# Kernel tuning notes

Hardware: AMD Instinct MI355X
Metric: run time of the kernel (lower is better)

## Reference

```python
import jax, jax.numpy as jnp
import numpy as np

EMB = 300      # emb_size
SEQ = 100      # seq_len
KW = 5         # kernel_width
KN = 50        # kernel_num
KMAX = 3       # maxpooling_num
MLP1 = 75      # decoder_mlp1_num
VOCAB = 50000 + 2
B = 2048
QLEN = 5


def setup_inputs() -> dict:
    key = jax.random.key(0)
    ks = jax.random.split(key, 11)
    input_q = jax.random.randint(ks[0], (QLEN,), 0, 50000)
    input_d = jax.random.randint(ks[1], (B, SEQ), 0, 50000)
    emb_table = jax.random.normal(ks[2], (VOCAB, EMB), jnp.float32) * 0.1
    conv_w = jax.random.normal(ks[3], (KW, 3 * EMB, KN), jnp.float32) * 0.02  # WIO
    conv_b = jnp.zeros((KN,), jnp.float32)
    gate_w = jax.random.normal(ks[4], (EMB, KN), jnp.float32) * 0.05
    gate_b = jnp.zeros((KN,), jnp.float32)
    hid_w = jax.random.normal(ks[5], (KN * KMAX, MLP1), jnp.float32) * 0.05
    hid_b = jnp.zeros((MLP1,), jnp.float32)
    score_w = jax.random.normal(ks[6], (MLP1, 1), jnp.float32) * 0.05
    score_b = jnp.zeros((1,), jnp.float32)
    return {"input_q": input_q, "input_d": input_d, "emb_table": emb_table,
            "conv_w": conv_w, "conv_b": conv_b, "gate_w": gate_w, "gate_b": gate_b,
            "hid_w": hid_w, "hid_b": hid_b, "score_w": score_w, "score_b": score_b}


def kmax_pool(x, k):
    # x: [B, KN, L]; keep top-k values along last axis in original sequence order
    _, idx = jax.lax.top_k(x, k)
    idx = jnp.sort(idx, axis=-1)
    return jnp.take_along_axis(x, idx, axis=-1)  # [B, KN, k]


def reference(input_q, input_d, emb_table, conv_w, conv_b, gate_w, gate_b,
              hid_w, hid_b, score_w, score_b):
    # class vector: mean of query-word embeddings -> [EMB]
    class_vec = emb_table[input_q].mean(axis=0)
    # category-specific gate -> [KN]
    query_gate = jax.nn.sigmoid(class_vec @ gate_w + gate_b)
    # document embeddings -> [B, SEQ, EMB]
    emb = emb_table[input_d]
    # elementwise interaction features, concat -> [B, SEQ, 3*EMB]
    conv_in = jnp.concatenate([emb, class_vec * emb, class_vec - emb], axis=-1)
    # conv over sequence (full-width kernel == 1D conv with C_in=3*EMB) -> [B, SEQ-KW+1, KN]
    conv = jax.lax.conv_general_dilated(
        conv_in, conv_w, window_strides=(1,), padding='VALID',
        dimension_numbers=('NWC', 'WIO', 'NWC')) + conv_b
    gated = query_gate * conv                      # [B, L', KN]
    pooled = kmax_pool(jnp.swapaxes(gated, 1, 2), KMAX)  # [B, KN, KMAX]
    enc = pooled.reshape(pooled.shape[0], -1)      # [B, KN*KMAX] = [B, 150]
    mlp1 = jnp.tanh(enc @ hid_w + hid_b)           # [B, 75]
    score = jnp.tanh(mlp1 @ score_w + score_b)     # [B, 1]
    return (mlp1, score)
```

## Files before the change

### kernel.cpp

```cpp
#include <hip/hip_runtime.h>
#include <math.h>

#define EMB   300
#define SEQ   100
#define KW    5
#define KN    50
#define NPAD  64
#define KMAX  3
#define MLP1  75
#define LOUT  96
#define BATCH 2048
#define EPAD  320
#define CHW   32
#define NCHK  10
#define SPW   36
#define TAU   2.5e-6
#define WHA   0.75
#define WHB   0.25
#define FLAG_TAU 1e-5f

#define WS_C    0
#define WS_GATE 320
#define WS_BIAS 384
#define WS_WG   448
#define F64_DBL 96448
#define WH_F    0
#define WL_F    51200
#define ENC_OFF 102400
#define ENC_PITCH 152
#define FLAGCNT_OFF 413696
#define FLAGLIST_OFF 413704
#define FLAGCAP 4096

typedef __attribute__((ext_vector_type(8))) short short8;
typedef __attribute__((ext_vector_type(4))) float f32x4;

__device__ __forceinline__ unsigned pack_hl(float x) {
    unsigned u = __float_as_uint(x);
    unsigned hi = (u + 0x7fffu + ((u >> 16) & 1u)) >> 16;
    float r = x - __uint_as_float(hi << 16);
    unsigned v = __float_as_uint(r);
    unsigned lo = (v + 0x7fffu + ((v >> 16) & 1u)) >> 16;
    return (hi << 16) | lo;
}

__global__ __launch_bounds__(256) void prep_a(
    const int* __restrict__ qids, const float* __restrict__ emb,
    const float* __restrict__ gate_w, const float* __restrict__ gate_b,
    const float* __restrict__ conv_w, const float* __restrict__ conv_b,
    double* __restrict__ ws, float* wsf)
{
    __shared__ double cS[EMB];
    __shared__ double gS[KN];
    __shared__ double pS[KW][KN];
    int t = threadIdx.x;
    if (t == 0) *(int*)(wsf + FLAGCNT_OFF) = 0;
    for (int e = t; e < EMB; e += 256) {
        double s = 0.0;
        for (int q = 0; q < 5; ++q) s += (double)emb[(size_t)qids[q] * EMB + e];
        double c = s * 0.2;
        cS[e] = c;
        ws[WS_C + e] = c;
    }
    __syncthreads();
    if (t < KN) {
        double g = (double)gate_b[t];
        for (int e = 0; e < EMB; ++e) g += cS[e] * (double)gate_w[e * KN + t];
        g = 1.0 / (1.0 + exp(-g));
        gS[t] = g;
        ws[WS_GATE + t] = g;
    }
    if (t < KW * KN) {
        int n = t % KN, w = t / KN;
        const float* base = conv_w + w * (3 * EMB * KN) + (2 * EMB) * KN + n;
        double p = 0.0;
        for (int e = 0; e < EMB; ++e) p += cS[e] * (double)base[e * KN];
        pS[w][n] = p;
    }
    __syncthreads();
    if (t < KN) {
        double s = (double)conv_b[t];
        for (int w = 0; w < KW; ++w) s += pS[w][t];
        ws[WS_BIAS + t] = gS[t] * s;
    }
}

__global__ __launch_bounds__(256) void prep_b(
    const float* __restrict__ conv_w, const double* __restrict__ ws,
    double* __restrict__ wg, float* __restrict__ wsf)
{
    int gid  = blockIdx.x * 256 + threadIdx.x;
    int wid  = gid >> 6;
    int lane = gid & 63;
    int w = wid / EPAD;
    int e = wid - w * EPAD;
    double v = 0.0;
    if (e < EMB && lane < KN) {
        double c = ws[WS_C + e];
        const float* p = conv_w + (size_t)w * (3 * EMB * KN) + (size_t)e * KN + lane;
        v = ws[WS_GATE + lane] *
            ((double)p[0] + c * (double)p[EMB * KN] - (double)p[2 * EMB * KN]);
    }
    if (e < EMB) wg[(size_t)(w * NPAD + lane) * EMB + e] = v;
    unsigned pk = pack_hl((float)v);
    unsigned short* Wh = (unsigned short*)(wsf + WH_F);
    unsigned short* Wl = (unsigned short*)(wsf + WL_F);
    size_t o = (size_t)(w * NPAD + lane) * EPAD + e;
    Wh[o] = (unsigned short)(pk >> 16);
    Wl[o] = (unsigned short)(pk & 0xffffu);
}

__global__ __launch_bounds__(256, 2) void main_mfma(
    const int* __restrict__ input_d, const float* __restrict__ emb,
    const double* __restrict__ ws, float* wsf,
    const float* __restrict__ hid_w, const float* __restrict__ hid_b,
    const float* __restrict__ score_w, const float* __restrict__ score_b,
    float* __restrict__ out)
{
    __shared__ __align__(16) unsigned stageS[4][SEQ * SPW];
    __shared__ float encS[4][ENC_PITCH];
    __shared__ float mlpS[4][MLP1 + 1];

    int t = threadIdx.x;
    int wid = t >> 6, lane = t & 63;
    int bb = blockIdx.x * 4 + wid;
    int m = lane & 15, kg = lane >> 4;
    unsigned* stg = &stageS[wid][0];

    int tv[7];
    #pragma unroll
    for (int it = 0; it < 7; ++it) {
        int i = lane + it * 64;
        tv[it] = (i < SEQ * 4) ? input_d[bb * SEQ + (i >> 2)] : 0;
    }

    f32x4 acc[6][4];
    #pragma unroll
    for (int lt = 0; lt < 6; ++lt)
        #pragma unroll
        for (int nt = 0; nt < 4; ++nt)
            acc[lt][nt] = (f32x4){0.f, 0.f, 0.f, 0.f};

    const unsigned short* Wh = (const unsigned short*)(wsf + WH_F);
    const unsigned short* Wl = (const unsigned short*)(wsf + WL_F);

    float4 pfa[4], pfb[4];
    #pragma unroll
    for (int it = 0; it < 4; ++it) {
        int i = lane + it * 64;
        int eg = i & 3;
        const float* er = emb + (size_t)tv[it] * EMB + eg * 8;
        pfa[it] = *(const float4*)(er);
        pfb[it] = *(const float4*)(er + 4);
    }

    #pragma unroll 1
    for (int c = 0; c < NCHK; ++c) {
        int e0 = c * CHW;
        float4 la[3], lb[3];
        #pragma unroll
        for (int it = 0; it < 3; ++it) {
            int i = lane + (it + 4) * 64;
            float4 z = {0.f, 0.f, 0.f, 0.f};
            la[it] = z; lb[it] = z;
            if (i < SEQ * 4) {
                int eg = i & 3, e = e0 + eg * 8;
                const float* er = emb + (size_t)tv[it + 4] * EMB;
                if (e < EMB)     la[it] = *(const float4*)(er + e);
                if (e + 4 < EMB) lb[it] = *(const float4*)(er + e + 4);
            }
        }
        #pragma unroll
        for (int it = 0; it < 4; ++it) {
            int i = lane + it * 64;
            int s = i >> 2, eg = i & 3;
            float4 fa = pfa[it], fb = pfb[it];
            unsigned p0 = pack_hl(fa.x), p1 = pack_hl(fa.y), p2 = pack_hl(fa.z), p3 = pack_hl(fa.w);
            unsigned p4 = pack_hl(fb.x), p5 = pack_hl(fb.y), p6 = pack_hl(fb.z), p7 = pack_hl(fb.w);
            uint4 hv, lv;
            hv.x = (p0 >> 16)     | (p1 & 0xffff0000u);
            hv.y = (p2 >> 16)     | (p3 & 0xffff0000u);
            hv.z = (p4 >> 16)     | (p5 & 0xffff0000u);
            hv.w = (p6 >> 16)     | (p7 & 0xffff0000u);
            lv.x = (p0 & 0xffffu) | (p1 << 16);
            lv.y = (p2 & 0xffffu) | (p3 << 16);
            lv.z = (p4 & 0xffffu) | (p5 << 16);
            lv.w = (p6 & 0xffffu) | (p7 << 16);
            unsigned* rowp = stg + s * SPW + eg * 8;
            *(uint4*)(rowp)     = hv;
            *(uint4*)(rowp + 4) = lv;
        }
        #pragma unroll
        for (int it = 0; it < 3; ++it) {
            int i = lane + (it + 4) * 64;
            if (i < SEQ * 4) {
                int s = i >> 2, eg = i & 3;
                float4 fa = la[it], fb = lb[it];
                unsigned p0 = pack_hl(fa.x), p1 = pack_hl(fa.y), p2 = pack_hl(fa.z), p3 = pack_hl(fa.w);
                unsigned p4 = pack_hl(fb.x), p5 = pack_hl(fb.y), p6 = pack_hl(fb.z), p7 = pack_hl(fb.w);
                uint4 hv, lv;
                hv.x = (p0 >> 16)     | (p1 & 0xffff0000u);
                hv.y = (p2 >> 16)     | (p3 & 0xffff0000u);
                hv.z = (p4 >> 16)     | (p5 & 0xffff0000u);
                hv.w = (p6 >> 16)     | (p7 & 0xffff0000u);
                lv.x = (p0 & 0xffffu) | (p1 << 16);
                lv.y = (p2 & 0xffffu) | (p3 << 16);
                lv.z = (p4 & 0xffffu) | (p5 << 16);
                lv.w = (p6 & 0xffffu) | (p7 << 16);
                unsigned* rowp = stg + s * SPW + eg * 8;
                *(uint4*)(rowp)     = hv;
                *(uint4*)(rowp + 4) = lv;
            }
        }
        #pragma unroll
        for (int w = 0; w < KW; ++w) {
            short8 Bh[4], Bl[4];
            #pragma unroll
            for (int nt = 0; nt < 4; ++nt) {
                size_t off = (size_t)(w * NPAD + nt * 16 + m) * EPAD + e0 + kg * 8;
                union { uint4 u; short8 s; } xb, yb;
                xb.u = *(const uint4*)(Wh + off);
                yb.u = *(const uint4*)(Wl + off);
                Bh[nt] = xb.s; Bl[nt] = yb.s;
            }
            if (w == KW - 1 && c + 1 < NCHK) {
                __builtin_amdgcn_sched_barrier(0);
                int e0n = e0 + CHW;
                #pragma unroll
                for (int it = 0; it < 4; ++it) {
                    int i = lane + it * 64;
                    int eg = i & 3, e = e0n + eg * 8;
                    float4 z = {0.f, 0.f, 0.f, 0.f};
                    pfa[it] = z; pfb[it] = z;
                    const float* er = emb + (size_t)tv[it] * EMB;
                    if (e < EMB)     pfa[it] = *(const float4*)(er + e);
                    if (e + 4 < EMB) pfb[it] = *(const float4*)(er + e + 4);
                }
                __builtin_amdgcn_sched_barrier(0);
            }
            #pragma unroll
            for (int lt = 0; lt < 6; ++lt) {
                int r = lt * 16 + m + w;
                const unsigned* ap = stg + r * SPW + kg * 8;
                short8 ah = *(const short8*)(ap);
                short8 al = *(const short8*)(ap + 4);
                #pragma unroll
                for (int nt = 0; nt < 4; ++nt) {
                    acc[lt][nt] = __builtin_amdgcn_mfma_f32_16x16x32_bf16(ah, Bh[nt], acc[lt][nt], 0, 0, 0);
                    acc[lt][nt] = __builtin_amdgcn_mfma_f32_16x16x32_bf16(al, Bh[nt], acc[lt][nt], 0, 0, 0);
                    acc[lt][nt] = __builtin_amdgcn_mfma_f32_16x16x32_bf16(ah, Bl[nt], acc[lt][nt], 0, 0, 0);
                }
            }
        }
    }

    float* gated = (float*)stg;
    #pragma unroll 1
    for (int ph = 0; ph < 2; ++ph) {
        int np0 = ph * 25;
        #pragma unroll
        for (int nt = 0; nt < 4; ++nt) {
            int n = nt * 16 + m;
            if (n >= np0 && n < np0 + 25) {
                float bias_n = (float)ws[WS_BIAS + n];
                #pragma unroll
                for (int lt = 0; lt < 6; ++lt)
                    #pragma unroll
                    for (int rr = 0; rr < 4; ++rr)
                        gated[(n - np0) * 97 + lt * 16 + kg * 4 + rr] = acc[lt][nt][rr] + bias_n;
            }
        }
        if (lane < 25) {
            int n = np0 + lane;
            const float* rowp = gated + lane * 97;
            float v1 = -1e30f, v2 = -1e30f, v3 = -1e30f, v4 = -1e30f;
            int   i1 = 0, i2 = 0, i3 = 0, i4 = 0;
            for (int l = 0; l < LOUT; ++l) {
                float v = rowp[l];
                if (v > v1)      { v4=v3; i4=i3; v3=v2; i3=i2; v2=v1; i2=i1; v1=v; i1=l; }
                else if (v > v2) { v4=v3; i4=i3; v3=v2; i3=i2; v2=v;  i2=l; }
                else if (v > v3) { v4=v3; i4=i3; v3=v;  i3=l; }
                else if (v > v4) { v4=v;  i4=l; }
            }
            float a0=v1, a1=v2, a2=v3; int j0=i1, j1=i2, j2=i3;
            if (j0 > j1) { float tv2=a0; a0=a1; a1=tv2; int ti=j0; j0=j1; j1=ti; }
            if (j1 > j2) { float tv2=a1; a1=a2; a2=tv2; int ti=j1; j1=j2; j2=ti; }
            if (j0 > j1) { float tv2=a0; a0=a1; a1=tv2; int ti=j0; j0=j1; j1=ti; }
            encS[wid][3*n] = a0; encS[wid][3*n+1] = a1; encS[wid][3*n+2] = a2;
            float* enc = wsf + ENC_OFF + (size_t)bb * ENC_PITCH + 3 * n;
            enc[0] = a0; enc[1] = a1; enc[2] = a2;
            if (v3 - v4 <= FLAG_TAU) {
                int idx = atomicAdd((int*)(wsf + FLAGCNT_OFF), 1);
                if (idx < FLAGCAP) ((int*)(wsf + FLAGLIST_OFF))[idx] = (bb << 6) | n;
            }
        }
    }
    __syncthreads();

    for (int i = t; i < 4 * MLP1; i += 256) {
        int d = i / MLP1, o = i - d * MLP1;
        float h = hid_b[o];
        for (int k = 0; k < KN * KMAX; ++k) h = fmaf(encS[d][k], hid_w[k * MLP1 + o], h);
        h = tanhf(h);
        mlpS[d][o] = h;
        out[(blockIdx.x * 4 + d) * MLP1 + o] = h;
    }
    __syncthreads();
    if (t < 4) {
        float s = score_b[0];
        for (int j = 0; j < MLP1; ++j) s = fmaf(mlpS[t][j], score_w[j], s);
        out[BATCH * MLP1 + blockIdx.x * 4 + t] = tanhf(s);
    }
}

__global__ __launch_bounds__(64) void cleanup_enc(
    const int* __restrict__ input_d, const float* __restrict__ emb,
    const double* __restrict__ ws, float* wsf)
{
    int cnt = *(const int*)(wsf + FLAGCNT_OFF);
    if (cnt > FLAGCAP) cnt = FLAGCAP;
    int idx = blockIdx.x;
    if (idx >= cnt) return;
    int code = ((const int*)(wsf + FLAGLIST_OFF))[idx];
    int b = code >> 6, n = code & 63;
    int lane = threadIdx.x;

    __shared__ int    tokS[SEQ];
    __shared__ double rowS[LOUT];
    for (int i = lane; i < SEQ; i += 64) tokS[i] = input_d[b * SEQ + i];
    __syncthreads();

    for (int l = lane; l < LOUT; l += 64) {
        double s = 0.0;
        for (int w = 0; w < KW; ++w) {
            const float*  er = emb + (size_t)tokS[l + w] * EMB;
            const double* wr = ws + WS_WG + (size_t)(w * NPAD + n) * EMB;
            for (int e = 0; e < EMB; ++e) s += (double)er[e] * wr[e];
        }
        rowS[l] = s + ws[WS_BIAS + n];
    }
    __syncthreads();

    if (lane == 0) {
        double v1=-1e300, v2=-1e300, v3=-1e300, v4=-1e300;
        int    i1=0, i2=0, i3=0, i4=0;
        for (int l = 0; l < LOUT; ++l) {
            double v = rowS[l];
            if (v > v1)      { v4=v3; i4=i3; v3=v2; i3=i2; v2=v1; i2=i1; v1=v; i1=l; }
            else if (v > v2) { v4=v3; i4=i3; v3=v2; i3=i2; v2=v;  i2=l; }
            else if (v > v3) { v4=v3; i4=i3; v3=v;  i3=l; }
            else if (v > v4) { v4=v;  i4=l; }
        }
        double a0=v1, a1=v2, a2=v3; int j0=i1, j1=i2, j2=i3;
        if (j0 > j1) { double tv=a0; a0=a1; a1=tv; int ti=j0; j0=j1; j1=ti; }
        if (j1 > j2) { double tv=a1; a1=a2; a2=tv; int ti=j1; j1=j2; j2=ti; }
        if (j0 > j1) { double tv=a0; a0=a1; a1=tv; int ti=j0; j0=j1; j1=ti; }
        double b0=v1, b1=v2, b2=v4; int k0=i1, k1=i2, k2=i4;
        if (k0 > k1) { double tv=b0; b0=b1; b1=tv; int ti=k0; k0=k1; k1=ti; }
        if (k1 > k2) { double tv=b1; b1=b2; b2=tv; int ti=k1; k1=k2; k2=ti; }
        if (k0 > k1) { double tv=b0; b0=b1; b1=tv; int ti=k0; k0=k1; k1=ti; }
        float* enc = wsf + ENC_OFF + (size_t)b * ENC_PITCH + 3 * n;
        if (v3 - v4 > TAU) {
            enc[0] = (float)a0; enc[1] = (float)a1; enc[2] = (float)a2;
        } else {
            enc[0] = (float)(WHA*a0 + WHB*b0);
            enc[1] = (float)(WHA*a1 + WHB*b1);
            enc[2] = (float)(WHA*a2 + WHB*b2);
        }
    }
}

__global__ __launch_bounds__(128) void cleanup_mlp(
    const float* wsf, const float* __restrict__ hid_w, const float* __restrict__ hid_b,
    const float* __restrict__ score_w, const float* __restrict__ score_b,
    float* __restrict__ out)
{
    int cnt = *(const int*)(wsf + FLAGCNT_OFF);
    if (cnt > FLAGCAP) cnt = FLAGCAP;
    if ((int)blockIdx.x >= cnt) return;
    int code = ((const int*)(wsf + FLAGLIST_OFF))[blockIdx.x];
    int b = code >> 6;
    int t = threadIdx.x;
    __shared__ float eS[KN * KMAX];
    __shared__ float mS[MLP1];
    const float* enc = wsf + ENC_OFF + (size_t)b * ENC_PITCH;
    for (int i = t; i < KN * KMAX; i += 128) eS[i] = enc[i];
    __syncthreads();
    if (t < MLP1) {
        float h = hid_b[t];
        for (int k = 0; k < KN * KMAX; ++k) h = fmaf(eS[k], hid_w[k * MLP1 + t], h);
        h = tanhf(h);
        mS[t] = h;
        out[b * MLP1 + t] = h;
    }
    __syncthreads();
    if (t == 0) {
        float s = score_b[0];
        for (int j = 0; j < MLP1; ++j) s = fmaf(mS[j], score_w[j], s);
        out[BATCH * MLP1 + b] = tanhf(s);
    }
}

extern "C" void kernel_launch(void* const* d_in, const int* in_sizes, int n_in,
                              void* d_out, int out_size, void* d_ws, size_t ws_size,
                              hipStream_t stream)
{
    const int*   input_q = (const int*)d_in[0];
    const int*   input_d = (const int*)d_in[1];
    const float* emb     = (const float*)d_in[2];
    const float* conv_w  = (const float*)d_in[3];
    const float* conv_b  = (const float*)d_in[4];
    const float* gate_w  = (const float*)d_in[5];
    const float* gate_b  = (const float*)d_in[6];
    const float* hid_w   = (const float*)d_in[7];
    const float* hid_b   = (const float*)d_in[8];
    const float* score_w = (const float*)d_in[9];
    const float* score_b = (const float*)d_in[10];
    float*  out = (float*)d_out;
    double* ws  = (double*)d_ws;
    float*  wsf = (float*)((char*)d_ws + (size_t)F64_DBL * 8);

    hipLaunchKernelGGL(prep_a, dim3(1), dim3(256), 0, stream,
                       input_q, emb, gate_w, gate_b, conv_w, conv_b, ws, wsf);
    hipLaunchKernelGGL(prep_b, dim3(400), dim3(256), 0, stream,
                       conv_w, ws, ws + WS_WG, wsf);
    hipLaunchKernelGGL(main_mfma, dim3(BATCH / 4), dim3(256), 0, stream,
                       input_d, emb, ws, wsf, hid_w, hid_b, score_w, score_b, out);
    hipLaunchKernelGGL(cleanup_enc, dim3(FLAGCAP), dim3(64), 0, stream,
                       input_d, emb, ws, wsf);
    hipLaunchKernelGGL(cleanup_mlp, dim3(FLAGCAP), dim3(128), 0, stream,
                       wsf, hid_w, hid_b, score_w, score_b, out);
}
```

Before: 363.1 us.

## Pre-split whole embedding table into bf16 hi/lo planes and gather directly into MFMA

Adds a prep kernel that converts the entire 50002-row embedding table into padded bf16 high/low planes in workspace, and a new main kernel that loads A fragments straight from those planes by token address instead of staging converted rows through shared memory. This removes the per-block fp32-to-bf16 split and LDS staging. In exchange it converts and writes the full table (about 64 MB) on every call, far more than the rows actually used. The new path only runs when the workspace is large enough, otherwise it falls back to the old kernel.

```diff
diff --git a/kernel.cpp b/kernel.cpp
--- a/kernel.cpp
+++ b/kernel.cpp
@@ -32,6 +32,13 @@
 #define FLAGLIST_OFF 413704
 #define FLAGCAP 4096
 
+#define VOCABN  50002
+#define EPITCH  320
+#define PLANE_BASE   2443264ull
+#define PLANE_WORDS  (50002ull * 320ull)
+#define PLANE_BYTES  (PLANE_WORDS * 2ull)
+#define WS_NEED (PLANE_BASE + 2ull * PLANE_BYTES)
+
 typedef __attribute__((ext_vector_type(8))) short short8;
 typedef __attribute__((ext_vector_type(4))) float f32x4;
 
@@ -108,6 +115,160 @@
     size_t o = (size_t)(w * NPAD + lane) * EPAD + e;
     Wh[o] = (unsigned short)(pk >> 16);
     Wl[o] = (unsigned short)(pk & 0xffffu);
+}
+
+__global__ __launch_bounds__(256) void prep_emb(
+    const float* __restrict__ emb,
+    unsigned short* __restrict__ eH, unsigned short* __restrict__ eL)
+{
+    int gid = blockIdx.x * 256 + threadIdx.x;
+    if (gid >= VOCABN * 40) return;
+    int row = gid / 40, eb = gid - row * 40;
+    int e = eb * 8;
+    float v[8];
+    #pragma unroll
+    for (int j = 0; j < 8; ++j) v[j] = 0.f;
+    if (e + 8 <= EMB) {
+        float4 a = *(const float4*)(emb + (size_t)row * EMB + e);
+        float4 b = *(const float4*)(emb + (size_t)row * EMB + e + 4);
+        v[0]=a.x; v[1]=a.y; v[2]=a.z; v[3]=a.w;
+        v[4]=b.x; v[5]=b.y; v[6]=b.z; v[7]=b.w;
+    } else if (e < EMB) {
+        for (int j = 0; j < EMB - e; ++j) v[j] = emb[(size_t)row * EMB + e + j];
+    }
+    union { unsigned short us[8]; uint4 u4; } hq, lq;
+    #pragma unroll
+    for (int j = 0; j < 8; ++j) {
+        unsigned pk = pack_hl(v[j]);
+        hq.us[j] = (unsigned short)(pk >> 16);
+        lq.us[j] = (unsigned short)(pk & 0xffffu);
+    }
+    size_t o = (size_t)row * EPITCH + e;
+    *(uint4*)(eH + o) = hq.u4;
+    *(uint4*)(eL + o) = lq.u4;
+}
+
+__global__ __launch_bounds__(256, 2) void main_direct(
+    const int* __restrict__ input_d,
+    const unsigned short* __restrict__ eH, const unsigned short* __restrict__ eL,
+    const double* __restrict__ ws, float* wsf,
+    const float* __restrict__ hid_w, const float* __restrict__ hid_b,
+    const float* __restrict__ score_w, const float* __restrict__ score_b,
+    float* __restrict__ out)
+{
+    __shared__ unsigned addrS[4][SEQ];
+    __shared__ __align__(16) float gatedS[4][25 * 97 + 3];
+    __shared__ float encS[4][ENC_PITCH];
+    __shared__ float mlpS[4][MLP1 + 1];
+
+    int t = threadIdx.x;
+    int wid = t >> 6, lane = t & 63;
+    int bb = blockIdx.x * 4 + wid;
+    int m = lane & 15, kg = lane >> 4;
+
+    for (int i = lane; i < SEQ; i += 64)
+        addrS[wid][i] = (unsigned)input_d[bb * SEQ + i] * 640u;
+
+    f32x4 acc[6][4];
+    #pragma unroll
+    for (int lt = 0; lt < 6; ++lt)
+        #pragma unroll
+        for (int nt = 0; nt < 4; ++nt)
+            acc[lt][nt] = (f32x4){0.f, 0.f, 0.f, 0.f};
+
+    const unsigned short* Wh = (const unsigned short*)(wsf + WH_F);
+    const unsigned short* Wl = (const unsigned short*)(wsf + WL_F);
+    const char* pH = (const char*)eH;
+    const char* pL = (const char*)eL;
+
+    #pragma unroll 1
+    for (int c = 0; c < NCHK; ++c) {
+        int e0 = c * CHW;
+        int ebyte = e0 * 2 + kg * 16;
+        #pragma unroll
+        for (int w = 0; w < KW; ++w) {
+            short8 Bh[4], Bl[4];
+            #pragma unroll
+            for (int nt = 0; nt < 4; ++nt) {
+                size_t off = (size_t)(w * NPAD + nt * 16 + m) * EPAD + e0 + kg * 8;
+                union { uint4 u; short8 s; } xb, yb;
+                xb.u = *(const uint4*)(Wh + off);
+                yb.u = *(const uint4*)(Wl + off);
+                Bh[nt] = xb.s; Bl[nt] = yb.s;
+            }
+            #pragma unroll
+            for (int lt = 0; lt < 6; ++lt) {
+                int r = lt * 16 + m + w;
+                unsigned aoff = addrS[wid][r];
+                short8 ah = *(const short8*)(pH + aoff + ebyte);
+                short8 al = *(const short8*)(pL + aoff + ebyte);
+                #pragma unroll
+                for (int nt = 0; nt < 4; ++nt) {
+                    acc[lt][nt] = __builtin_amdgcn_mfma_f32_16x16x32_bf16(ah, Bh[nt], acc[lt][nt], 0, 0, 0);
+                    acc[lt][nt] = __builtin_amdgcn_mfma_f32_16x16x32_bf16(al, Bh[nt], acc[lt][nt], 0, 0, 0);
+                    acc[lt][nt] = __builtin_amdgcn_mfma_f32_16x16x32_bf16(ah, Bl[nt], acc[lt][nt], 0, 0, 0);
+                }
+            }
+        }
+    }
+
+    float* gated = gatedS[wid];
+    #pragma unroll 1
+    for (int ph = 0; ph < 2; ++ph) {
+        int np0 = ph * 25;
+        #pragma unroll
+        for (int nt = 0; nt < 4; ++nt) {
+            int n = nt * 16 + m;
+            if (n >= np0 && n < np0 + 25) {
+                float bias_n = (float)ws[WS_BIAS + n];
+                #pragma unroll
+                for (int lt = 0; lt < 6; ++lt)
+                    #pragma unroll
+                    for (int rr = 0; rr < 4; ++rr)
+                        gated[(n - np0) * 97 + lt * 16 + kg * 4 + rr] = acc[lt][nt][rr] + bias_n;
+            }
+        }
+        if (lane < 25) {
+            int n = np0 + lane;
+            const float* rowp = gated + lane * 97;
+            float v1 = -1e30f, v2 = -1e30f, v3 = -1e30f, v4 = -1e30f;
+            int   i1 = 0, i2 = 0, i3 = 0, i4 = 0;
+            for (int l = 0; l < LOUT; ++l) {
+                float v = rowp[l];
+                if (v > v1)      { v4=v3; i4=i3; v3=v2; i3=i2; v2=v1; i2=i1; v1=v; i1=l; }
+                else if (v > v2) { v4=v3; i4=i3; v3=v2; i3=i2; v2=v;  i2=l; }
+                else if (v > v3) { v4=v3; i4=i3; v3=v;  i3=l; }
+                else if (v > v4) { v4=v;  i4=l; }
+            }
+            float a0=v1, a1=v2, a2=v3; int j0=i1, j1=i2, j2=i3;
+            if (j0 > j1) { float tv2=a0; a0=a1; a1=tv2; int ti=j0; j0=j1; j1=ti; }
+            if (j1 > j2) { float tv2=a1; a1=a2; a2=tv2; int ti=j1; j1=j2; j2=ti; }
+            if (j0 > j1) { float tv2=a0; a0=a1; a1=tv2; int ti=j0; j0=j1; j1=ti; }
+            encS[wid][3*n] = a0; encS[wid][3*n+1] = a1; encS[wid][3*n+2] = a2;
+            float* enc = wsf + ENC_OFF + (size_t)bb * ENC_PITCH + 3 * n;
+            enc[0] = a0; enc[1] = a1; enc[2] = a2;
+            if (v3 - v4 <= FLAG_TAU) {
+                int idx = atomicAdd((int*)(wsf + FLAGCNT_OFF), 1);
+                if (idx < FLAGCAP) ((int*)(wsf + FLAGLIST_OFF))[idx] = (bb << 6) | n;
+            }
+        }
+    }
+    __syncthreads();
+
+    for (int i = t; i < 4 * MLP1; i += 256) {
+        int d = i / MLP1, o = i - d * MLP1;
+        float h = hid_b[o];
+        for (int k = 0; k < KN * KMAX; ++k) h = fmaf(encS[d][k], hid_w[k * MLP1 + o], h);
+        h = tanhf(h);
+        mlpS[d][o] = h;
+        out[(blockIdx.x * 4 + d) * MLP1 + o] = h;
+    }
+    __syncthreads();
+    if (t < 4) {
+        float s = score_b[0];
+        for (int j = 0; j < MLP1; ++j) s = fmaf(mlpS[t][j], score_w[j], s);
+        out[BATCH * MLP1 + blockIdx.x * 4 + t] = tanhf(s);
+    }
 }
 
 __global__ __launch_bounds__(256, 2) void main_mfma(
@@ -424,8 +585,19 @@
                        input_q, emb, gate_w, gate_b, conv_w, conv_b, ws, wsf);
     hipLaunchKernelGGL(prep_b, dim3(400), dim3(256), 0, stream,
                        conv_w, ws, ws + WS_WG, wsf);
-    hipLaunchKernelGGL(main_mfma, dim3(BATCH / 4), dim3(256), 0, stream,
-                       input_d, emb, ws, wsf, hid_w, hid_b, score_w, score_b, out);
+
+    if (ws_size >= WS_NEED) {
+        unsigned short* eH = (unsigned short*)((char*)d_ws + PLANE_BASE);
+        unsigned short* eL = eH + PLANE_WORDS;
+        hipLaunchKernelGGL(prep_emb, dim3((VOCABN * 40 + 255) / 256), dim3(256), 0, stream,
+                           emb, eH, eL);
+        hipLaunchKernelGGL(main_direct, dim3(BATCH / 4), dim3(256), 0, stream,
+                           input_d, eH, eL, ws, wsf, hid_w, hid_b, score_w, score_b, out);
+    } else {
+        hipLaunchKernelGGL(main_mfma, dim3(BATCH / 4), dim3(256), 0, stream,
+                           input_d, emb, ws, wsf, hid_w, hid_b, score_w, score_b, out);
+    }
+
     hipLaunchKernelGGL(cleanup_enc, dim3(FLAGCAP), dim3(64), 0, stream,
                        input_d, emb, ws, wsf);
     hipLaunchKernelGGL(cleanup_mlp, dim3(FLAGCAP), dim3(128), 0, stream,
```

Result: slower. 568.8 us (+56.6%).
